# Optimization experiments

Hardware: AMD Instinct MI355X
Metric: run time of the kernel (lower is better)

Reference implementation:

```python
import jax, jax.numpy as jnp
import numpy as np

N = 40000      # nodes
E = 640000     # edges
IN_DIM = 128
HID = 128
HEADS = 4
DHEAD = HID // HEADS  # 32
LAYERS = 3
TIMESTEPS = 2
NEG_SLOPE = 0.2


def setup_inputs() -> dict:
    key = jax.random.key(0)
    ks = jax.random.split(key, 16)
    s = 0.05
    inp = {
        "node_feats": jax.random.normal(ks[0], (N, IN_DIM), jnp.float32),
        "src": jax.random.randint(ks[1], (E,), 0, N, jnp.int32),
        "dst": jax.random.randint(ks[2], (E,), 0, N, jnp.int32),
        "proj_W": jax.random.normal(ks[3], (IN_DIM, HID), jnp.float32) * s,
        "proj_b": jnp.zeros((HID,), jnp.float32),
        "fc_W": jax.random.normal(ks[4], (LAYERS, HID, HID), jnp.float32) * s,
        "attn_l": jax.random.normal(ks[5], (LAYERS, HEADS, DHEAD), jnp.float32) * s,
        "attn_r": jax.random.normal(ks[6], (LAYERS, HEADS, DHEAD), jnp.float32) * s,
        "conv_bias": jnp.zeros((LAYERS, HID), jnp.float32),
        "gru_Wih": jax.random.normal(ks[7], (3 * HID, HID), jnp.float32) * s,
        "gru_Whh": jax.random.normal(ks[8], (3 * HID, HID), jnp.float32) * s,
        "gru_bih": jnp.zeros((3 * HID,), jnp.float32),
        "gru_bhh": jnp.zeros((3 * HID,), jnp.float32),
    }
    return inp


def _gat_layer(h, src, dst, fc_W, attn_l, attn_r, bias):
    # h: (N, HID). DGL GATConv: fc -> edge attn -> segment softmax -> scatter sum
    feat = (h @ fc_W).reshape(N, HEADS, DHEAD)
    el = jnp.einsum('nhd,hd->nh', feat, attn_l)  # (N, H)
    er = jnp.einsum('nhd,hd->nh', feat, attn_r)
    e = jax.nn.leaky_relu(el[src] + er[dst], NEG_SLOPE)  # (E, H)
    # segment softmax over incoming edges per destination node
    emax = jax.ops.segment_max(e, dst, num_segments=N)  # (N, H)
    ee = jnp.exp(e - emax[dst])
    denom = jax.ops.segment_sum(ee, dst, num_segments=N)
    alpha = ee / denom[dst]  # (E, H)
    msg = feat[src] * alpha[:, :, None]  # (E, H, D)
    rst = jax.ops.segment_sum(msg, dst, num_segments=N)  # (N, H, D)
    rst = rst + h.reshape(N, HEADS, DHEAD)          # identity residual
    rst = rst + bias.reshape(HEADS, DHEAD)          # learned bias
    return jax.nn.elu(rst).reshape(N, HID)


def _gru_step(x, Wih, Whh, bih, bhh):
    # seq_len == 1, h0 == 0 -> recurrent matmul Whh @ h0 vanishes; b_hh remains
    gi = x @ Wih.T + bih  # (N, 3*HID)
    r = jax.nn.sigmoid(gi[:, :HID] + bhh[:HID])
    z = jax.nn.sigmoid(gi[:, HID:2 * HID] + bhh[HID:2 * HID])
    n = jnp.tanh(gi[:, 2 * HID:] + r * bhh[2 * HID:])
    return (1.0 - z) * n


def reference(node_feats, src, dst, proj_W, proj_b, fc_W, attn_l, attn_r,
              conv_bias, gru_Wih, gru_Whh, gru_bih, gru_bhh):
    h = node_feats @ proj_W + proj_b
    for l in range(LAYERS):
        h = _gat_layer(h, src, dst, fc_W[l], attn_l[l], attn_r[l], conv_bias[l])
    for _ in range(TIMESTEPS):
        h = _gru_step(h, gru_Wih, gru_Whh, gru_bih, gru_bhh)
    return h
```

## Files before the change

### kernel.cpp

```cpp
#include <hip/hip_runtime.h>
#include <hip/hip_bf16.h>

#define NNODES 40000
#define NEDGES 640000
#define M2PAD  40064
#define HID    128
#define PADCAP 920064

typedef __attribute__((ext_vector_type(8))) short bf16x8;
typedef __attribute__((ext_vector_type(4))) float f32x4;

__device__ __forceinline__ float bl(unsigned u){ return __uint_as_float(u << 16); }
__device__ __forceinline__ float bh(unsigned u){ return __uint_as_float(u & 0xFFFF0000u); }
__device__ __forceinline__ unsigned short f2b(float f){
    unsigned u = __float_as_uint(f);
    u = (u + 0x7FFFu + ((u >> 16) & 1u)) >> 16;
    return (unsigned short)u;
}
__device__ __forceinline__ float fast_rcp(float x){ return __builtin_amdgcn_rcpf(x); }

__device__ __forceinline__ void g2l16(const void* g, void* l){
    __builtin_amdgcn_global_load_lds(
        (const __attribute__((address_space(1))) unsigned int*)g,
        (__attribute__((address_space(3))) unsigned int*)l, 16, 0, 0);
}

__device__ __forceinline__ float wcalc(float e, float erw, int j, int rem){
    float t = e + erw;
    t = (t > 0.f) ? t : 0.2f * t;
    t = __expf(t);
    return (j < rem) ? t : 0.f;
}

__device__ __forceinline__ unsigned lds_off(int row, int col){
    return (unsigned)(row * 256 + (((col >> 3) ^ (row & 15)) << 4) + ((col & 7) << 1));
}

__global__ void prep_all(const float* __restrict__ node_feats,
                         const float* __restrict__ proj_W, const float* __restrict__ fc_W,
                         const float* __restrict__ gru_Wih, const int* __restrict__ dstp,
                         unsigned short* __restrict__ nf,
                         unsigned short* __restrict__ projWT, unsigned short* __restrict__ fcWT,
                         unsigned short* __restrict__ gruWb, int* __restrict__ deg){
    int b = blockIdx.x;
    if (b < 5000){
        int gid = b * 256 + threadIdx.x;
        float4 v = ((const float4*)node_feats)[gid];
        ushort4 o;
        o.x = f2b(v.x); o.y = f2b(v.y); o.z = f2b(v.z); o.w = f2b(v.w);
        ((ushort4*)nf)[gid] = o;
    } else if (b < 5256){
        int t = b - 5000;
        int c = t >> 6;
        int idx = (t & 63) * 256 + threadIdx.x;
        const float* in   = (c == 0) ? proj_W : fc_W + (size_t)(c - 1) * 16384;
        unsigned short* o = (c == 0) ? projWT : fcWT + (size_t)(c - 1) * 16384;
        int k = idx >> 7, n = idx & 127;
        o[n * 128 + k] = f2b(in[idx]);
    } else if (b < 5448){
        int idx = (b - 5256) * 256 + threadIdx.x;
        gruWb[idx] = f2b(gru_Wih[idx]);
    } else {
        int e = (b - 5448) * 256 + threadIdx.x;
        atomicAdd(&deg[dstp[e]], 1);
    }
}

__global__ __launch_bounds__(1024) void scan_kernel(const int* __restrict__ deg,
        int* __restrict__ rowptr, int* __restrict__ cur, int Nn4){
    __shared__ int wsum[17];
    __shared__ int carry;
    int t = threadIdx.x, lane = t & 63, wid = t >> 6;
    if (t == 0) carry = 0;
    __syncthreads();
    for (int base = 0; base < Nn4; base += 1024){
        int i4 = base + t;
        int4 dg = (i4 < Nn4) ? ((const int4*)deg)[i4] : make_int4(0, 0, 0, 0);
        int p0 = (dg.x + 7) & ~7, p1 = (dg.y + 7) & ~7;
        int p2 = (dg.z + 7) & ~7, p3 = (dg.w + 7) & ~7;
        int v = p0 + p1 + p2 + p3;
        int x = v;
        #pragma unroll
        for (int d = 1; d < 64; d <<= 1){
            int y = __shfl_up(x, d, 64);
            if (lane >= d) x += y;
        }
        if (lane == 63) wsum[wid] = x;
        __syncthreads();
        if (wid == 0){
            int vv = (lane < 16) ? wsum[lane] : 0;
            int xx = vv;
            #pragma unroll
            for (int d = 1; d < 16; d <<= 1){
                int y = __shfl_up(xx, d, 64);
                if (lane >= d) xx += y;
            }
            if (lane < 16) wsum[lane] = xx - vv;
            if (lane == 15) wsum[16] = xx;
        }
        __syncthreads();
        int excl = carry + wsum[wid] + (x - v);
        if (i4 < Nn4){
            int4 o = make_int4(excl, excl + p0, excl + p0 + p1, excl + p0 + p1 + p2);
            ((int4*)rowptr)[i4] = o;
            ((int4*)cur)[i4]    = o;
        }
        __syncthreads();
        if (t == 0) carry += wsum[16];
        __syncthreads();
    }
    if (t == 0) rowptr[Nn4 * 4] = carry;
}

__global__ void fill_kernel(const int* __restrict__ src, const int* __restrict__ dst,
                            int* __restrict__ cur, int* __restrict__ esrc){
    int e = blockIdx.x * 256 + threadIdx.x;
    int d = dst[e];
    int pos = atomicAdd(&cur[d], 1);
    esrc[pos] = src[e];
}

template<int MT>
__global__ __launch_bounds__(256) void gemm_t(
        const unsigned short* __restrict__ A, const unsigned short* __restrict__ BT,
        const float* __restrict__ bias, void* __restrict__ C,
        int Mreal, int ldc, int outF32,
        const float* __restrict__ al, const float* __restrict__ ar,
        float* __restrict__ elp, float* __restrict__ erp)
{
    __shared__ unsigned char lds[MT * 256 + 32768];
    unsigned char* ldsA = lds;
    unsigned char* ldsB = lds + MT * 256;
    int w = threadIdx.x >> 6, lane = threadIdx.x & 63;
    int rsub = lane >> 4, c16 = lane & 15;
    long baseM = (long)blockIdx.x * MT;
    long baseN = (long)blockIdx.y * 128;

    #pragma unroll
    for (int i = 0; i < MT / 16; i++){
        int chunk = w * (MT / 16) + i;
        int r = chunk * 4 + rsub;
        int cg = c16 ^ (r & 15);
        long ar_ = baseM + r; if (ar_ >= Mreal) ar_ = Mreal - 1;
        g2l16((const unsigned char*)A + ar_ * 256 + cg * 16, ldsA + chunk * 1024);
    }
    #pragma unroll
    for (int i = 0; i < 8; i++){
        int chunk = w * 8 + i;
        int r = chunk * 4 + rsub;
        int cg = c16 ^ (r & 15);
        long br = baseN + r;
        g2l16((const unsigned char*)BT + br * 256 + cg * 16, ldsB + chunk * 1024);
    }
    __syncthreads();

    constexpr int MI = 4;
    constexpr int NI = (MT == 128) ? 4 : 2;
    int mo = (MT == 128) ? (w & 1) * 64 : 0;
    int no = (MT == 128) ? (w >> 1) * 64 : w * 32;
    int q = lane >> 4, cl = lane & 15;
    f32x4 acc[MI][NI];
    #pragma unroll
    for (int i = 0; i < MI; i++)
        #pragma unroll
        for (int j = 0; j < NI; j++) acc[i][j] = (f32x4){0.f, 0.f, 0.f, 0.f};

    #pragma unroll
    for (int kc = 0; kc < 4; kc++){
        bf16x8 av[MI], bv[NI];
        #pragma unroll
        for (int mi = 0; mi < MI; mi++){
            int row = mo + mi * 16 + cl;
            int cs = (kc * 4 + q) ^ (row & 15);
            av[mi] = *(const bf16x8*)(ldsA + row * 256 + cs * 16);
        }
        #pragma unroll
        for (int ni = 0; ni < NI; ni++){
            int row = no + ni * 16 + cl;
            int cs = (kc * 4 + q) ^ (row & 15);
            bv[ni] = *(const bf16x8*)(ldsB + row * 256 + cs * 16);
        }
        #pragma unroll
        for (int mi = 0; mi < MI; mi++)
            #pragma unroll
            for (int ni = 0; ni < NI; ni++)
                acc[mi][ni] = __builtin_amdgcn_mfma_f32_16x16x32_bf16(av[mi], bv[ni], acc[mi][ni], 0, 0, 0);
    }

    #pragma unroll
    for (int mi = 0; mi < MI; mi++){
        #pragma unroll
        for (int ni = 0; ni < NI; ni++){
            int gn = (int)baseN + no + ni * 16 + cl;
            float bvf = bias ? bias[gn] : 0.f;
            long gm0 = baseM + mo + mi * 16 + q * 4;
            #pragma unroll
            for (int reg = 0; reg < 4; reg++){
                float v = acc[mi][ni][reg] + bvf;
                long gm = gm0 + reg;
                if (gm < Mreal){
                    if (outF32) ((float*)C)[gm * ldc + gn] = v;
                    else ((unsigned short*)C)[gm * ldc + gn] = f2b(v);
                }
            }
        }
    }

    if (NI == 2 && al){
        float al_lo = al[no + cl], al_hi = al[no + 16 + cl];
        float ar_lo = ar[no + cl], ar_hi = ar[no + 16 + cl];
        #pragma unroll
        for (int mi = 0; mi < MI; mi++){
            #pragma unroll
            for (int reg = 0; reg < 4; reg++){
                float pl = acc[mi][0][reg] * al_lo + acc[mi][1][reg] * al_hi;
                float pr = acc[mi][0][reg] * ar_lo + acc[mi][1][reg] * ar_hi;
                #pragma unroll
                for (int msk = 8; msk; msk >>= 1){
                    pl += __shfl_xor(pl, msk, 64);
                    pr += __shfl_xor(pr, msk, 64);
                }
                long gm = baseM + mi * 16 + q * 4 + reg;
                if (cl == 0 && gm < Mreal){
                    elp[gm * 4 + w] = pl;
                    erp[gm * 4 + w] = pr;
                }
            }
        }
    }
}

__global__ __launch_bounds__(256) void proj_fc1(
        const unsigned short* __restrict__ nf,
        const unsigned short* __restrict__ projWT, const float* __restrict__ proj_b,
        const unsigned short* __restrict__ fcWT0,
        unsigned short* __restrict__ h, unsigned short* __restrict__ feat,
        const float* __restrict__ al, const float* __restrict__ ar,
        float* __restrict__ elp, float* __restrict__ erp)
{
    __shared__ unsigned char ldsA[16384];
    __shared__ unsigned char ldsB[32768];
    int w = threadIdx.x >> 6, lane = threadIdx.x & 63;
    int rsub = lane >> 4, c16 = lane & 15;
    long baseM = (long)blockIdx.x * 64;

    #pragma unroll
    for (int i = 0; i < 4; i++){
        int chunk = w * 4 + i;
        int r = chunk * 4 + rsub;
        int cg = c16 ^ (r & 15);
        g2l16((const unsigned char*)nf + (baseM + r) * 256 + cg * 16, ldsA + chunk * 1024);
    }
    #pragma unroll
    for (int i = 0; i < 8; i++){
        int chunk = w * 8 + i;
        int r = chunk * 4 + rsub;
        int cg = c16 ^ (r & 15);
        g2l16((const unsigned char*)projWT + r * 256 + cg * 16, ldsB + chunk * 1024);
    }
    __syncthreads();

    int no = w * 32;
    int q = lane >> 4, cl = lane & 15;
    f32x4 acc[4][2];
    #pragma unroll
    for (int i = 0; i < 4; i++)
        #pragma unroll
        for (int j = 0; j < 2; j++) acc[i][j] = (f32x4){0.f, 0.f, 0.f, 0.f};

    #pragma unroll
    for (int kc = 0; kc < 4; kc++){
        bf16x8 av[4], bv[2];
        #pragma unroll
        for (int mi = 0; mi < 4; mi++){
            int row = mi * 16 + cl;
            int cs = (kc * 4 + q) ^ (row & 15);
            av[mi] = *(const bf16x8*)(ldsA + row * 256 + cs * 16);
        }
        #pragma unroll
        for (int ni = 0; ni < 2; ni++){
            int row = no + ni * 16 + cl;
            int cs = (kc * 4 + q) ^ (row & 15);
            bv[ni] = *(const bf16x8*)(ldsB + row * 256 + cs * 16);
        }
        #pragma unroll
        for (int mi = 0; mi < 4; mi++)
            #pragma unroll
            for (int ni = 0; ni < 2; ni++)
                acc[mi][ni] = __builtin_amdgcn_mfma_f32_16x16x32_bf16(av[mi], bv[ni], acc[mi][ni], 0, 0, 0);
    }
    __syncthreads();

    #pragma unroll
    for (int ni = 0; ni < 2; ni++){
        int j = no + ni * 16 + cl;
        float bvf = proj_b[j];
        #pragma unroll
        for (int mi = 0; mi < 4; mi++){
            #pragma unroll
            for (int reg = 0; reg < 4; reg++){
                int row = mi * 16 + q * 4 + reg;
                unsigned short bb = f2b(acc[mi][ni][reg] + bvf);
                h[(baseM + row) * 128 + j] = bb;
                *(unsigned short*)(ldsA + lds_off(row, j)) = bb;
            }
        }
    }
    #pragma unroll
    for (int i = 0; i < 8; i++){
        int chunk = w * 8 + i;
        int r = chunk * 4 + rsub;
        int cg = c16 ^ (r & 15);
        g2l16((const unsigned char*)fcWT0 + r * 256 + cg * 16, ldsB + chunk * 1024);
    }
    __syncthreads();

    #pragma unroll
    for (int i = 0; i < 4; i++)
        #pragma unroll
        for (int j = 0; j < 2; j++) acc[i][j] = (f32x4){0.f, 0.f, 0.f, 0.f};

    #pragma unroll
    for (int kc = 0; kc < 4; kc++){
        bf16x8 av[4], bv[2];
        #pragma unroll
        for (int mi = 0; mi < 4; mi++){
            int row = mi * 16 + cl;
            int cs = (kc * 4 + q) ^ (row & 15);
            av[mi] = *(const bf16x8*)(ldsA + row * 256 + cs * 16);
        }
        #pragma unroll
        for (int ni = 0; ni < 2; ni++){
            int row = no + ni * 16 + cl;
            int cs = (kc * 4 + q) ^ (row & 15);
            bv[ni] = *(const bf16x8*)(ldsB + row * 256 + cs * 16);
        }
        #pragma unroll
        for (int mi = 0; mi < 4; mi++)
            #pragma unroll
            for (int ni = 0; ni < 2; ni++)
                acc[mi][ni] = __builtin_amdgcn_mfma_f32_16x16x32_bf16(av[mi], bv[ni], acc[mi][ni], 0, 0, 0);
    }

    #pragma unroll
    for (int mi = 0; mi < 4; mi++){
        #pragma unroll
        for (int ni = 0; ni < 2; ni++){
            int gn = no + ni * 16 + cl;
            #pragma unroll
            for (int reg = 0; reg < 4; reg++){
                long gm = baseM + mi * 16 + q * 4 + reg;
                feat[gm * 128 + gn] = f2b(acc[mi][ni][reg]);
            }
        }
    }
    float al_lo = al[no + cl], al_hi = al[no + 16 + cl];
    float ar_lo = ar[no + cl], ar_hi = ar[no + 16 + cl];
    #pragma unroll
    for (int mi = 0; mi < 4; mi++){
        #pragma unroll
        for (int reg = 0; reg < 4; reg++){
            float pl = acc[mi][0][reg] * al_lo + acc[mi][1][reg] * al_hi;
            float pr = acc[mi][0][reg] * ar_lo + acc[mi][1][reg] * ar_hi;
            #pragma unroll
            for (int msk = 8; msk; msk >>= 1){
                pl += __shfl_xor(pl, msk, 64);
                pr += __shfl_xor(pr, msk, 64);
            }
            long gm = baseM + mi * 16 + q * 4 + reg;
            if (cl == 0){
                elp[gm * 4 + w] = pl;
                erp[gm * 4 + w] = pr;
            }
        }
    }
}

__global__ __launch_bounds__(256) void gru2x(
        const unsigned short* __restrict__ A, const unsigned short* __restrict__ BT,
        const float* __restrict__ bih, const float* __restrict__ bhh,
        float* __restrict__ out, int Mreal)
{
    __shared__ unsigned char ldsA[16384];
    __shared__ unsigned char ldsB[32768];
    int w = threadIdx.x >> 6, lane = threadIdx.x & 63;
    int rsub = lane >> 4, c16 = lane & 15;
    long baseM = (long)blockIdx.x * 64;

    #pragma unroll
    for (int i = 0; i < 4; i++){
        int chunk = w * 4 + i;
        int r = chunk * 4 + rsub;
        int cg = c16 ^ (r & 15);
        g2l16((const unsigned char*)A + (baseM + r) * 256 + cg * 16, ldsA + chunk * 1024);
    }

    int no = w * 32;
    int q = lane >> 4, cl = lane & 15;
    f32x4 acc[3][4][2];

    #pragma unroll
    for (int s = 0; s < 2; s++){
        #pragma unroll
        for (int c = 0; c < 3; c++)
            #pragma unroll
            for (int i = 0; i < 4; i++)
                #pragma unroll
                for (int j = 0; j < 2; j++) acc[c][i][j] = (f32x4){0.f, 0.f, 0.f, 0.f};

        #pragma unroll
        for (int c = 0; c < 3; c++){
            __syncthreads();
            #pragma unroll
            for (int i = 0; i < 8; i++){
                int chunk = w * 8 + i;
                int r = chunk * 4 + rsub;
                int cg = c16 ^ (r & 15);
                long br = c * 128 + r;
                g2l16((const unsigned char*)BT + br * 256 + cg * 16, ldsB + chunk * 1024);
            }
            __syncthreads();
            #pragma unroll
            for (int kc = 0; kc < 4; kc++){
                bf16x8 av[4], bv[2];
                #pragma unroll
                for (int mi = 0; mi < 4; mi++){
                    int row = mi * 16 + cl;
                    int cs = (kc * 4 + q) ^ (row & 15);
                    av[mi] = *(const bf16x8*)(ldsA + row * 256 + cs * 16);
                }
                #pragma unroll
                for (int ni = 0; ni < 2; ni++){
                    int row = no + ni * 16 + cl;
                    int cs = (kc * 4 + q) ^ (row & 15);
                    bv[ni] = *(const bf16x8*)(ldsB + row * 256 + cs * 16);
                }
                #pragma unroll
                for (int mi = 0; mi < 4; mi++)
                    #pragma unroll
                    for (int ni = 0; ni < 2; ni++)
                        acc[c][mi][ni] = __builtin_amdgcn_mfma_f32_16x16x32_bf16(av[mi], bv[ni], acc[c][mi][ni], 0, 0, 0);
            }
        }
        if (s == 0) __syncthreads();

        #pragma unroll
        for (int ni = 0; ni < 2; ni++){
            int j = no + ni * 16 + cl;
            float bir = bih[j]       + bhh[j];
            float biz = bih[128 + j] + bhh[128 + j];
            float bin = bih[256 + j];
            float bhn = bhh[256 + j];
            #pragma unroll
            for (int mi = 0; mi < 4; mi++){
                #pragma unroll
                for (int reg = 0; reg < 4; reg++){
                    int row = mi * 16 + q * 4 + reg;
                    float gr = acc[0][mi][ni][reg] + bir;
                    float gz = acc[1][mi][ni][reg] + biz;
                    float gn = acc[2][mi][ni][reg] + bin;
                    float r = fast_rcp(1.f + __expf(-gr));
                    float z = fast_rcp(1.f + __expf(-gz));
                    float ex = __expf(2.f * (gn + r * bhn));
                    float nn = (ex - 1.f) * fast_rcp(ex + 1.f);
                    float v = (1.f - z) * nn;
                    if (s == 0){
                        *(unsigned short*)(ldsA + lds_off(row, j)) = f2b(v);
                    } else {
                        long nr = baseM + row;
                        if (nr < Mreal) out[nr * 128 + j] = v;
                    }
                }
            }
        }
    }
}

__global__ __launch_bounds__(256) void aggregate(
        const int* __restrict__ rowptr, const int* __restrict__ degv,
        const int* __restrict__ esrc,
        const float* __restrict__ el, const float* __restrict__ er,
        const unsigned short* __restrict__ feat, const float* __restrict__ bias,
        unsigned short* __restrict__ h)
{
    int wid = threadIdx.x >> 6, lane = threadIdx.x & 63;
    int n = blockIdx.x * 4 + wid;
    int hh = lane >> 4;
    int d0 = lane * 2;
    unsigned doff = (unsigned)(d0 * 2);
    int beg = rowptr[n], end = rowptr[n + 1];
    int dg  = degv[n];
    float erw = er[(size_t)n * 4 + hh];
    float s = 0.f, a0 = 0.f, a1 = 0.f;
    const char* fbc = (const char*)feat;
    const int*  ep  = esrc + beg;

    if (beg < end){
        int4 sA = *(const int4*)(ep);
        int4 sB = *(const int4*)(ep + 4);
        float e0=0.f,e1=0.f,e2=0.f,e3=0.f,e4=0.f,e5=0.f,e6=0.f,e7=0.f;
        unsigned f0=0,f1=0,f2=0,f3=0,f4=0,f5=0,f6=0,f7=0;
        int rprev = 0;
        int rcur  = dg;
        for (int p = beg; p < end; p += 8){
            float g0 = el[(((unsigned)sA.x) << 2) + hh];
            float g1 = el[(((unsigned)sA.y) << 2) + hh];
            float g2 = el[(((unsigned)sA.z) << 2) + hh];
            float g3 = el[(((unsigned)sA.w) << 2) + hh];
            float g4 = el[(((unsigned)sB.x) << 2) + hh];
            float g5 = el[(((unsigned)sB.y) << 2) + hh];
            float g6 = el[(((unsigned)sB.z) << 2) + hh];
            float g7 = el[(((unsigned)sB.w) << 2) + hh];
            unsigned c0 = *(const unsigned*)(fbc + ((((unsigned)sA.x) << 8) + doff));
            unsigned c1 = *(const unsigned*)(fbc + ((((unsigned)sA.y) << 8) + doff));
            unsigned c2 = *(const unsigned*)(fbc + ((((unsigned)sA.z) << 8) + doff));
            unsigned c3 = *(const unsigned*)(fbc + ((((unsigned)sA.w) << 8) + doff));
            unsigned c4 = *(const unsigned*)(fbc + ((((unsigned)sB.x) << 8) + doff));
            unsigned c5 = *(const unsigned*)(fbc + ((((unsigned)sB.y) << 8) + doff));
            unsigned c6 = *(const unsigned*)(fbc + ((((unsigned)sB.z) << 8) + doff));
            unsigned c7 = *(const unsigned*)(fbc + ((((unsigned)sB.w) << 8) + doff));
            int4 nA = *(const int4*)(ep + 8);
            int4 nB = *(const int4*)(ep + 12);
            float w0 = wcalc(e0, erw, 0, rprev);
            float w1 = wcalc(e1, erw, 1, rprev);
            float w2 = wcalc(e2, erw, 2, rprev);
            float w3 = wcalc(e3, erw, 3, rprev);
            float w4 = wcalc(e4, erw, 4, rprev);
            float w5 = wcalc(e5, erw, 5, rprev);
            float w6 = wcalc(e6, erw, 6, rprev);
            float w7 = wcalc(e7, erw, 7, rprev);
            s += ((w0 + w1) + (w2 + w3)) + ((w4 + w5) + (w6 + w7));
            a0 = fmaf(w0, bl(f0), fmaf(w1, bl(f1), fmaf(w2, bl(f2), fmaf(w3, bl(f3), a0))));
            a0 = fmaf(w4, bl(f4), fmaf(w5, bl(f5), fmaf(w6, bl(f6), fmaf(w7, bl(f7), a0))));
            a1 = fmaf(w0, bh(f0), fmaf(w1, bh(f1), fmaf(w2, bh(f2), fmaf(w3, bh(f3), a1))));
            a1 = fmaf(w4, bh(f4), fmaf(w5, bh(f5), fmaf(w6, bh(f6), fmaf(w7, bh(f7), a1))));
            e0 = g0; e1 = g1; e2 = g2; e3 = g3; e4 = g4; e5 = g5; e6 = g6; e7 = g7;
            f0 = c0; f1 = c1; f2 = c2; f3 = c3; f4 = c4; f5 = c5; f6 = c6; f7 = c7;
            sA = nA; sB = nB;
            rprev = rcur; rcur -= 8;
            ep += 8;
        }
        float w0 = wcalc(e0, erw, 0, rprev);
        float w1 = wcalc(e1, erw, 1, rprev);
        float w2 = wcalc(e2, erw, 2, rprev);
        float w3 = wcalc(e3, erw, 3, rprev);
        float w4 = wcalc(e4, erw, 4, rprev);
        float w5 = wcalc(e5, erw, 5, rprev);
        float w6 = wcalc(e6, erw, 6, rprev);
        float w7 = wcalc(e7, erw, 7, rprev);
        s += ((w0 + w1) + (w2 + w3)) + ((w4 + w5) + (w6 + w7));
        a0 = fmaf(w0, bl(f0), fmaf(w1, bl(f1), fmaf(w2, bl(f2), fmaf(w3, bl(f3), a0))));
        a0 = fmaf(w4, bl(f4), fmaf(w5, bl(f5), fmaf(w6, bl(f6), fmaf(w7, bl(f7), a0))));
        a1 = fmaf(w0, bh(f0), fmaf(w1, bh(f1), fmaf(w2, bh(f2), fmaf(w3, bh(f3), a1))));
        a1 = fmaf(w4, bh(f4), fmaf(w5, bh(f5), fmaf(w6, bh(f6), fmaf(w7, bh(f7), a1))));
    }
    float inv = (s > 0.f) ? fast_rcp(s) : 0.f;
    unsigned hv = *(const unsigned*)(h + (size_t)n * 128 + d0);
    float x0 = a0 * inv + bl(hv) + bias[d0];
    float x1 = a1 * inv + bh(hv) + bias[d0 + 1];
    x0 = (x0 > 0.f) ? x0 : expm1f(x0);
    x1 = (x1 > 0.f) ? x1 : expm1f(x1);
    unsigned outv = (unsigned)f2b(x0) | ((unsigned)f2b(x1) << 16);
    *(unsigned*)(h + (size_t)n * 128 + d0) = outv;
}

extern "C" void kernel_launch(void* const* d_in, const int* in_sizes, int n_in,
                              void* d_out, int out_size, void* d_ws, size_t ws_size,
                              hipStream_t stream) {
    const float* node_feats = (const float*)d_in[0];
    const int*   srcp       = (const int*)d_in[1];
    const int*   dstp       = (const int*)d_in[2];
    const float* proj_W     = (const float*)d_in[3];
    const float* proj_b     = (const float*)d_in[4];
    const float* fc_W       = (const float*)d_in[5];
    const float* attn_l     = (const float*)d_in[6];
    const float* attn_r     = (const float*)d_in[7];
    const float* conv_bias  = (const float*)d_in[8];
    const float* gru_Wih    = (const float*)d_in[9];
    const float* gru_bih    = (const float*)d_in[11];
    const float* gru_bhh    = (const float*)d_in[12];
    float* outp = (float*)d_out;

    char* ws = (char*)d_ws;
    size_t off = 0;
    auto carve = [&](size_t bytes) -> char* {
        char* p = ws + off;
        off += (bytes + 255) & ~(size_t)255;
        return p;
    };
    int*            deg    = (int*)carve((size_t)NNODES * 4);
    int*            rowptr = (int*)carve((size_t)(NNODES + 1) * 4);
    int*            cur    = (int*)carve((size_t)NNODES * 4);
    int*            esrc   = (int*)carve((size_t)(PADCAP + 32) * 4);
    float*          el     = (float*)carve((size_t)NNODES * 4 * 4);
    float*          er     = (float*)carve((size_t)NNODES * 4 * 4);
    unsigned short* projWT = (unsigned short*)carve(16384 * 2);
    unsigned short* fcWT   = (unsigned short*)carve(3 * 16384 * 2);
    unsigned short* gruWb  = (unsigned short*)carve(49152 * 2);
    unsigned short* nf     = (unsigned short*)carve((size_t)NNODES * 128 * 2);
    unsigned short* h      = (unsigned short*)carve((size_t)M2PAD * 128 * 2);
    unsigned short* feat   = (unsigned short*)carve((size_t)M2PAD * 128 * 2);
    (void)ws_size; (void)in_sizes; (void)n_in; (void)out_size;

    hipMemsetAsync(deg, 0, (size_t)NNODES * 4, stream);
    hipMemsetAsync(esrc, 0, (size_t)(PADCAP + 32) * 4, stream);
    prep_all<<<7948, 256, 0, stream>>>(node_feats, proj_W, fc_W, gru_Wih, dstp,
                                       nf, projWT, fcWT, gruWb, deg);
    scan_kernel<<<1, 1024, 0, stream>>>(deg, rowptr, cur, NNODES / 4);
    fill_kernel<<<NEDGES / 256, 256, 0, stream>>>(srcp, dstp, cur, esrc);

    proj_fc1<<<625, 256, 0, stream>>>(nf, projWT, proj_b, fcWT, h, feat,
                                      attn_l, attn_r, el, er);

    for (int l = 0; l < 3; l++){
        if (l > 0){
            gemm_t<64><<<dim3(625, 1), 256, 0, stream>>>(h, fcWT + l * 16384, nullptr, feat, NNODES, 128, 0,
                                                         attn_l + l * 128, attn_r + l * 128, el, er);
        }
        aggregate<<<NNODES / 4, 256, 0, stream>>>(rowptr, deg, esrc, el, er, feat,
                                                  conv_bias + l * 128, h);
    }

    gru2x<<<625, 256, 0, stream>>>(h, gruWb, gru_bih, gru_bhh, outp, NNODES);
}
```

Measured before the change: 361.8 us.

## Split degree atomics into 8 sub-counters and load GEMM operands directly from global

Degree counting and CSR fill now spread their atomics across 8 sub-counter arrays chosen by edge index, which cuts contention on hot destination nodes. The scan merges these into per-node totals and per-slot offsets. The GEMM, proj_fc1 and GRU kernels drop the LDS staging through global_load_lds and read A and B fragments straight from global memory, removing barriers and LDS traffic at the cost of redundant, uncoalesced global reads. The two memsets are merged into one, and the row bounds checks are removed because the grid covers exactly the node count.

```diff
diff --git a/kernel.cpp b/kernel.cpp
--- a/kernel.cpp
+++ b/kernel.cpp
@@ -19,12 +19,6 @@
 }
 __device__ __forceinline__ float fast_rcp(float x){ return __builtin_amdgcn_rcpf(x); }
 
-__device__ __forceinline__ void g2l16(const void* g, void* l){
-    __builtin_amdgcn_global_load_lds(
-        (const __attribute__((address_space(1))) unsigned int*)g,
-        (__attribute__((address_space(3))) unsigned int*)l, 16, 0, 0);
-}
-
 __device__ __forceinline__ float wcalc(float e, float erw, int j, int rem){
     float t = e + erw;
     t = (t > 0.f) ? t : 0.2f * t;
@@ -41,7 +35,7 @@
                          const float* __restrict__ gru_Wih, const int* __restrict__ dstp,
                          unsigned short* __restrict__ nf,
                          unsigned short* __restrict__ projWT, unsigned short* __restrict__ fcWT,
-                         unsigned short* __restrict__ gruWb, int* __restrict__ deg){
+                         unsigned short* __restrict__ gruWb, int* __restrict__ deg8){
     int b = blockIdx.x;
     if (b < 5000){
         int gid = b * 256 + threadIdx.x;
@@ -62,12 +56,12 @@
         gruWb[idx] = f2b(gru_Wih[idx]);
     } else {
         int e = (b - 5448) * 256 + threadIdx.x;
-        atomicAdd(&deg[dstp[e]], 1);
-    }
-}
-
-__global__ __launch_bounds__(1024) void scan_kernel(const int* __restrict__ deg,
-        int* __restrict__ rowptr, int* __restrict__ cur, int Nn4){
+        atomicAdd(&deg8[(e & 7) * NNODES + dstp[e]], 1);
+    }
+}
+
+__global__ __launch_bounds__(1024) void scan_kernel(const int* __restrict__ deg8,
+        int* __restrict__ rowptr, int* __restrict__ degt, int* __restrict__ cur8, int Nn4){
     __shared__ int wsum[17];
     __shared__ int carry;
     int t = threadIdx.x, lane = t & 63, wid = t >> 6;
@@ -75,15 +69,22 @@
     __syncthreads();
     for (int base = 0; base < Nn4; base += 1024){
         int i4 = base + t;
-        int4 dg = (i4 < Nn4) ? ((const int4*)deg)[i4] : make_int4(0, 0, 0, 0);
-        int p0 = (dg.x + 7) & ~7, p1 = (dg.y + 7) & ~7;
-        int p2 = (dg.z + 7) & ~7, p3 = (dg.w + 7) & ~7;
+        int4 d[8];
+        #pragma unroll
+        for (int x = 0; x < 8; x++)
+            d[x] = (i4 < Nn4) ? ((const int4*)(deg8 + (size_t)x * NNODES))[i4]
+                              : make_int4(0, 0, 0, 0);
+        int s0 = 0, s1 = 0, s2 = 0, s3 = 0;
+        #pragma unroll
+        for (int x = 0; x < 8; x++){ s0 += d[x].x; s1 += d[x].y; s2 += d[x].z; s3 += d[x].w; }
+        int p0 = (s0 + 7) & ~7, p1 = (s1 + 7) & ~7;
+        int p2 = (s2 + 7) & ~7, p3 = (s3 + 7) & ~7;
         int v = p0 + p1 + p2 + p3;
         int x = v;
         #pragma unroll
-        for (int d = 1; d < 64; d <<= 1){
-            int y = __shfl_up(x, d, 64);
-            if (lane >= d) x += y;
+        for (int dd = 1; dd < 64; dd <<= 1){
+            int y = __shfl_up(x, dd, 64);
+            if (lane >= dd) x += y;
         }
         if (lane == 63) wsum[wid] = x;
         __syncthreads();
@@ -91,9 +92,9 @@
             int vv = (lane < 16) ? wsum[lane] : 0;
             int xx = vv;
             #pragma unroll
-            for (int d = 1; d < 16; d <<= 1){
-                int y = __shfl_up(xx, d, 64);
-                if (lane >= d) xx += y;
+            for (int dd = 1; dd < 16; dd <<= 1){
+                int y = __shfl_up(xx, dd, 64);
+                if (lane >= dd) xx += y;
             }
             if (lane < 16) wsum[lane] = xx - vv;
             if (lane == 15) wsum[16] = xx;
@@ -103,7 +104,13 @@
         if (i4 < Nn4){
             int4 o = make_int4(excl, excl + p0, excl + p0 + p1, excl + p0 + p1 + p2);
             ((int4*)rowptr)[i4] = o;
-            ((int4*)cur)[i4]    = o;
+            ((int4*)degt)[i4]   = make_int4(s0, s1, s2, s3);
+            int o0 = o.x, o1 = o.y, o2 = o.z, o3 = o.w;
+            #pragma unroll
+            for (int xx2 = 0; xx2 < 8; xx2++){
+                ((int4*)(cur8 + (size_t)xx2 * NNODES))[i4] = make_int4(o0, o1, o2, o3);
+                o0 += d[xx2].x; o1 += d[xx2].y; o2 += d[xx2].z; o3 += d[xx2].w;
+            }
         }
         __syncthreads();
         if (t == 0) carry += wsum[16];
@@ -113,118 +120,77 @@
 }
 
 __global__ void fill_kernel(const int* __restrict__ src, const int* __restrict__ dst,
-                            int* __restrict__ cur, int* __restrict__ esrc){
+                            int* __restrict__ cur8, int* __restrict__ esrc){
     int e = blockIdx.x * 256 + threadIdx.x;
     int d = dst[e];
-    int pos = atomicAdd(&cur[d], 1);
+    int pos = atomicAdd(&cur8[(e & 7) * NNODES + d], 1);
     esrc[pos] = src[e];
 }
 
-template<int MT>
 __global__ __launch_bounds__(256) void gemm_t(
         const unsigned short* __restrict__ A, const unsigned short* __restrict__ BT,
-        const float* __restrict__ bias, void* __restrict__ C,
-        int Mreal, int ldc, int outF32,
+        unsigned short* __restrict__ C,
         const float* __restrict__ al, const float* __restrict__ ar,
         float* __restrict__ elp, float* __restrict__ erp)
 {
-    __shared__ unsigned char lds[MT * 256 + 32768];
-    unsigned char* ldsA = lds;
-    unsigned char* ldsB = lds + MT * 256;
     int w = threadIdx.x >> 6, lane = threadIdx.x & 63;
-    int rsub = lane >> 4, c16 = lane & 15;
-    long baseM = (long)blockIdx.x * MT;
-    long baseN = (long)blockIdx.y * 128;
-
-    #pragma unroll
-    for (int i = 0; i < MT / 16; i++){
-        int chunk = w * (MT / 16) + i;
-        int r = chunk * 4 + rsub;
-        int cg = c16 ^ (r & 15);
-        long ar_ = baseM + r; if (ar_ >= Mreal) ar_ = Mreal - 1;
-        g2l16((const unsigned char*)A + ar_ * 256 + cg * 16, ldsA + chunk * 1024);
-    }
-    #pragma unroll
-    for (int i = 0; i < 8; i++){
-        int chunk = w * 8 + i;
-        int r = chunk * 4 + rsub;
-        int cg = c16 ^ (r & 15);
-        long br = baseN + r;
-        g2l16((const unsigned char*)BT + br * 256 + cg * 16, ldsB + chunk * 1024);
-    }
-    __syncthreads();
-
-    constexpr int MI = 4;
-    constexpr int NI = (MT == 128) ? 4 : 2;
-    int mo = (MT == 128) ? (w & 1) * 64 : 0;
-    int no = (MT == 128) ? (w >> 1) * 64 : w * 32;
+    long baseM = (long)blockIdx.x * 64;
+    int no = w * 32;
     int q = lane >> 4, cl = lane & 15;
-    f32x4 acc[MI][NI];
-    #pragma unroll
-    for (int i = 0; i < MI; i++)
-        #pragma unroll
-        for (int j = 0; j < NI; j++) acc[i][j] = (f32x4){0.f, 0.f, 0.f, 0.f};
+    const unsigned short* Ab = A + baseM * 128;
+
+    f32x4 acc[4][2];
+    #pragma unroll
+    for (int i = 0; i < 4; i++)
+        #pragma unroll
+        for (int j = 0; j < 2; j++) acc[i][j] = (f32x4){0.f, 0.f, 0.f, 0.f};
 
     #pragma unroll
     for (int kc = 0; kc < 4; kc++){
-        bf16x8 av[MI], bv[NI];
-        #pragma unroll
-        for (int mi = 0; mi < MI; mi++){
-            int row = mo + mi * 16 + cl;
-            int cs = (kc * 4 + q) ^ (row & 15);
-            av[mi] = *(const bf16x8*)(ldsA + row * 256 + cs * 16);
-        }
-        #pragma unroll
-        for (int ni = 0; ni < NI; ni++){
-            int row = no + ni * 16 + cl;
-            int cs = (kc * 4 + q) ^ (row & 15);
-            bv[ni] = *(const bf16x8*)(ldsB + row * 256 + cs * 16);
-        }
-        #pragma unroll
-        for (int mi = 0; mi < MI; mi++)
-            #pragma unroll
-            for (int ni = 0; ni < NI; ni++)
+        int co = kc * 32 + q * 8;
+        bf16x8 av[4], bv[2];
+        #pragma unroll
+        for (int mi = 0; mi < 4; mi++)
+            av[mi] = *(const bf16x8*)(Ab + (mi * 16 + cl) * 128 + co);
+        #pragma unroll
+        for (int ni = 0; ni < 2; ni++)
+            bv[ni] = *(const bf16x8*)(BT + (no + ni * 16 + cl) * 128 + co);
+        #pragma unroll
+        for (int mi = 0; mi < 4; mi++)
+            #pragma unroll
+            for (int ni = 0; ni < 2; ni++)
                 acc[mi][ni] = __builtin_amdgcn_mfma_f32_16x16x32_bf16(av[mi], bv[ni], acc[mi][ni], 0, 0, 0);
     }
 
     #pragma unroll
-    for (int mi = 0; mi < MI; mi++){
-        #pragma unroll
-        for (int ni = 0; ni < NI; ni++){
-            int gn = (int)baseN + no + ni * 16 + cl;
-            float bvf = bias ? bias[gn] : 0.f;
-            long gm0 = baseM + mo + mi * 16 + q * 4;
-            #pragma unroll
-            for (int reg = 0; reg < 4; reg++){
-                float v = acc[mi][ni][reg] + bvf;
-                long gm = gm0 + reg;
-                if (gm < Mreal){
-                    if (outF32) ((float*)C)[gm * ldc + gn] = v;
-                    else ((unsigned short*)C)[gm * ldc + gn] = f2b(v);
-                }
-            }
-        }
-    }
-
-    if (NI == 2 && al){
-        float al_lo = al[no + cl], al_hi = al[no + 16 + cl];
-        float ar_lo = ar[no + cl], ar_hi = ar[no + 16 + cl];
-        #pragma unroll
-        for (int mi = 0; mi < MI; mi++){
-            #pragma unroll
-            for (int reg = 0; reg < 4; reg++){
-                float pl = acc[mi][0][reg] * al_lo + acc[mi][1][reg] * al_hi;
-                float pr = acc[mi][0][reg] * ar_lo + acc[mi][1][reg] * ar_hi;
-                #pragma unroll
-                for (int msk = 8; msk; msk >>= 1){
-                    pl += __shfl_xor(pl, msk, 64);
-                    pr += __shfl_xor(pr, msk, 64);
-                }
-                long gm = baseM + mi * 16 + q * 4 + reg;
-                if (cl == 0 && gm < Mreal){
-                    elp[gm * 4 + w] = pl;
-                    erp[gm * 4 + w] = pr;
-                }
+    for (int mi = 0; mi < 4; mi++){
+        #pragma unroll
+        for (int ni = 0; ni < 2; ni++){
+            int gn = no + ni * 16 + cl;
+            long gm0 = baseM + mi * 16 + q * 4;
+            #pragma unroll
+            for (int reg = 0; reg < 4; reg++)
+                C[(gm0 + reg) * 128 + gn] = f2b(acc[mi][ni][reg]);
+        }
+    }
+
+    float al_lo = al[no + cl], al_hi = al[no + 16 + cl];
+    float ar_lo = ar[no + cl], ar_hi = ar[no + 16 + cl];
+    #pragma unroll
+    for (int mi = 0; mi < 4; mi++){
+        #pragma unroll
+        for (int reg = 0; reg < 4; reg++){
+            float pl = acc[mi][0][reg] * al_lo + acc[mi][1][reg] * al_hi;
+            float pr = acc[mi][0][reg] * ar_lo + acc[mi][1][reg] * ar_hi;
+            #pragma unroll
+            for (int msk = 8; msk; msk >>= 1){
+                pl += __shfl_xor(pl, msk, 64);
+                pr += __shfl_xor(pr, msk, 64);
+            }
+            long gm = baseM + mi * 16 + q * 4 + reg;
+            if (cl == 0){
+                elp[gm * 4 + w] = pl;
+                erp[gm * 4 + w] = pr;
             }
         }
     }
@@ -239,29 +205,12 @@
         float* __restrict__ elp, float* __restrict__ erp)
 {
     __shared__ unsigned char ldsA[16384];
-    __shared__ unsigned char ldsB[32768];
     int w = threadIdx.x >> 6, lane = threadIdx.x & 63;
-    int rsub = lane >> 4, c16 = lane & 15;
     long baseM = (long)blockIdx.x * 64;
-
-    #pragma unroll
-    for (int i = 0; i < 4; i++){
-        int chunk = w * 4 + i;
-        int r = chunk * 4 + rsub;
-        int cg = c16 ^ (r & 15);
-        g2l16((const unsigned char*)nf + (baseM + r) * 256 + cg * 16, ldsA + chunk * 1024);
-    }
-    #pragma unroll
-    for (int i = 0; i < 8; i++){
-        int chunk = w * 8 + i;
-        int r = chunk * 4 + rsub;
-        int cg = c16 ^ (r & 15);
-        g2l16((const unsigned char*)projWT + r * 256 + cg * 16, ldsB + chunk * 1024);
-    }
-    __syncthreads();
-
     int no = w * 32;
     int q = lane >> 4, cl = lane & 15;
+    const unsigned short* Ab = nf + baseM * 256 / 2 * 2;
+
     f32x4 acc[4][2];
     #pragma unroll
     for (int i = 0; i < 4; i++)
@@ -270,26 +219,20 @@
 
     #pragma unroll
     for (int kc = 0; kc < 4; kc++){
+        int co = kc * 32 + q * 8;
         bf16x8 av[4], bv[2];
         #pragma unroll
-        for (int mi = 0; mi < 4; mi++){
-            int row = mi * 16 + cl;
-            int cs = (kc * 4 + q) ^ (row & 15);
-            av[mi] = *(const bf16x8*)(ldsA + row * 256 + cs * 16);
-        }
-        #pragma unroll
-        for (int ni = 0; ni < 2; ni++){
-            int row = no + ni * 16 + cl;
-            int cs = (kc * 4 + q) ^ (row & 15);
-            bv[ni] = *(const bf16x8*)(ldsB + row * 256 + cs * 16);
-        }
+        for (int mi = 0; mi < 4; mi++)
+            av[mi] = *(const bf16x8*)(nf + (baseM + mi * 16 + cl) * 128 + co);
+        #pragma unroll
+        for (int ni = 0; ni < 2; ni++)
+            bv[ni] = *(const bf16x8*)(projWT + (no + ni * 16 + cl) * 128 + co);
         #pragma unroll
         for (int mi = 0; mi < 4; mi++)
             #pragma unroll
             for (int ni = 0; ni < 2; ni++)
                 acc[mi][ni] = __builtin_amdgcn_mfma_f32_16x16x32_bf16(av[mi], bv[ni], acc[mi][ni], 0, 0, 0);
     }
-    __syncthreads();
 
     #pragma unroll
     for (int ni = 0; ni < 2; ni++){
@@ -306,13 +249,6 @@
             }
         }
     }
-    #pragma unroll
-    for (int i = 0; i < 8; i++){
-        int chunk = w * 8 + i;
-        int r = chunk * 4 + rsub;
-        int cg = c16 ^ (r & 15);
-        g2l16((const unsigned char*)fcWT0 + r * 256 + cg * 16, ldsB + chunk * 1024);
-    }
     __syncthreads();
 
     #pragma unroll
@@ -322,6 +258,7 @@
 
     #pragma unroll
     for (int kc = 0; kc < 4; kc++){
+        int co = kc * 32 + q * 8;
         bf16x8 av[4], bv[2];
         #pragma unroll
         for (int mi = 0; mi < 4; mi++){
@@ -330,11 +267,8 @@
             av[mi] = *(const bf16x8*)(ldsA + row * 256 + cs * 16);
         }
         #pragma unroll
-        for (int ni = 0; ni < 2; ni++){
-            int row = no + ni * 16 + cl;
-            int cs = (kc * 4 + q) ^ (row & 15);
-            bv[ni] = *(const bf16x8*)(ldsB + row * 256 + cs * 16);
-        }
+        for (int ni = 0; ni < 2; ni++)
+            bv[ni] = *(const bf16x8*)(fcWT0 + (no + ni * 16 + cl) * 128 + co);
         #pragma unroll
         for (int mi = 0; mi < 4; mi++)
             #pragma unroll
@@ -379,70 +313,58 @@
 __global__ __launch_bounds__(256) void gru2x(
         const unsigned short* __restrict__ A, const unsigned short* __restrict__ BT,
         const float* __restrict__ bih, const float* __restrict__ bhh,
-        float* __restrict__ out, int Mreal)
+        float* __restrict__ out)
 {
     __shared__ unsigned char ldsA[16384];
-    __shared__ unsigned char ldsB[32768];
     int w = threadIdx.x >> 6, lane = threadIdx.x & 63;
-    int rsub = lane >> 4, c16 = lane & 15;
     long baseM = (long)blockIdx.x * 64;
-
-    #pragma unroll
-    for (int i = 0; i < 4; i++){
-        int chunk = w * 4 + i;
-        int r = chunk * 4 + rsub;
-        int cg = c16 ^ (r & 15);
-        g2l16((const unsigned char*)A + (baseM + r) * 256 + cg * 16, ldsA + chunk * 1024);
-    }
-
     int no = w * 32;
     int q = lane >> 4, cl = lane & 15;
-    f32x4 acc[3][4][2];
 
     #pragma unroll
     for (int s = 0; s < 2; s++){
-        #pragma unroll
-        for (int c = 0; c < 3; c++)
-            #pragma unroll
-            for (int i = 0; i < 4; i++)
+        bf16x8 avall[4][4];
+        if (s == 0){
+            #pragma unroll
+            for (int kc = 0; kc < 4; kc++)
                 #pragma unroll
-                for (int j = 0; j < 2; j++) acc[c][i][j] = (f32x4){0.f, 0.f, 0.f, 0.f};
-
-        #pragma unroll
-        for (int c = 0; c < 3; c++){
+                for (int mi = 0; mi < 4; mi++)
+                    avall[kc][mi] = *(const bf16x8*)(A + (baseM + mi * 16 + cl) * 128 + kc * 32 + q * 8);
+        } else {
             __syncthreads();
             #pragma unroll
-            for (int i = 0; i < 8; i++){
-                int chunk = w * 8 + i;
-                int r = chunk * 4 + rsub;
-                int cg = c16 ^ (r & 15);
-                long br = c * 128 + r;
-                g2l16((const unsigned char*)BT + br * 256 + cg * 16, ldsB + chunk * 1024);
-            }
-            __syncthreads();
-            #pragma unroll
-            for (int kc = 0; kc < 4; kc++){
-                bf16x8 av[4], bv[2];
+            for (int kc = 0; kc < 4; kc++)
                 #pragma unroll
                 for (int mi = 0; mi < 4; mi++){
                     int row = mi * 16 + cl;
                     int cs = (kc * 4 + q) ^ (row & 15);
-                    av[mi] = *(const bf16x8*)(ldsA + row * 256 + cs * 16);
+                    avall[kc][mi] = *(const bf16x8*)(ldsA + row * 256 + cs * 16);
                 }
+        }
+
+        f32x4 acc[3][4][2];
+        #pragma unroll
+        for (int c = 0; c < 3; c++)
+            #pragma unroll
+            for (int i = 0; i < 4; i++)
                 #pragma unroll
-                for (int ni = 0; ni < 2; ni++){
-                    int row = no + ni * 16 + cl;
-                    int cs = (kc * 4 + q) ^ (row & 15);
-                    bv[ni] = *(const bf16x8*)(ldsB + row * 256 + cs * 16);
-                }
+                for (int j = 0; j < 2; j++) acc[c][i][j] = (f32x4){0.f, 0.f, 0.f, 0.f};
+
+        #pragma unroll
+        for (int c = 0; c < 3; c++){
+            #pragma unroll
+            for (int kc = 0; kc < 4; kc++){
+                bf16x8 bv[2];
+                #pragma unroll
+                for (int ni = 0; ni < 2; ni++)
+                    bv[ni] = *(const bf16x8*)(BT + (c * 128 + no + ni * 16 + cl) * 128 + kc * 32 + q * 8);
                 #pragma unroll
                 for (int mi = 0; mi < 4; mi++)
                     #pragma unroll
                     for (int ni = 0; ni < 2; ni++)
-                        acc[c][mi][ni] = __builtin_amdgcn_mfma_f32_16x16x32_bf16(av[mi], bv[ni], acc[c][mi][ni], 0, 0, 0);
-            }
-        }
-        if (s == 0) __syncthreads();
+                        acc[c][mi][ni] = __builtin_amdgcn_mfma_f32_16x16x32_bf16(avall[kc][mi], bv[ni], acc[c][mi][ni], 0, 0, 0);
+            }
+        }
 
         #pragma unroll
         for (int ni = 0; ni < 2; ni++){
@@ -464,12 +386,10 @@
                     float ex = __expf(2.f * (gn + r * bhn));
                     float nn = (ex - 1.f) * fast_rcp(ex + 1.f);
                     float v = (1.f - z) * nn;
-                    if (s == 0){
+                    if (s == 0)
                         *(unsigned short*)(ldsA + lds_off(row, j)) = f2b(v);
-                    } else {
-                        long nr = baseM + row;
-                        if (nr < Mreal) out[nr * 128 + j] = v;
-                    }
+                    else
+                        out[(baseM + row) * 128 + j] = v;
                 }
             }
         }
@@ -588,10 +508,11 @@
         off += (bytes + 255) & ~(size_t)255;
         return p;
     };
-    int*            deg    = (int*)carve((size_t)NNODES * 4);
+    int*            deg8   = (int*)carve((size_t)8 * NNODES * 4);
+    int*            esrc   = (int*)carve((size_t)(PADCAP + 32) * 4);
     int*            rowptr = (int*)carve((size_t)(NNODES + 1) * 4);
-    int*            cur    = (int*)carve((size_t)NNODES * 4);
-    int*            esrc   = (int*)carve((size_t)(PADCAP + 32) * 4);
+    int*            degt   = (int*)carve((size_t)NNODES * 4);
+    int*            cur8   = (int*)carve((size_t)8 * NNODES * 4);
     float*          el     = (float*)carve((size_t)NNODES * 4 * 4);
     float*          er     = (float*)carve((size_t)NNODES * 4 * 4);
     unsigned short* projWT = (unsigned short*)carve(16384 * 2);
@@ -602,24 +523,23 @@
     unsigned short* feat   = (unsigned short*)carve((size_t)M2PAD * 128 * 2);
     (void)ws_size; (void)in_sizes; (void)n_in; (void)out_size;
 
-    hipMemsetAsync(deg, 0, (size_t)NNODES * 4, stream);
-    hipMemsetAsync(esrc, 0, (size_t)(PADCAP + 32) * 4, stream);
+    hipMemsetAsync(deg8, 0, (size_t)8 * NNODES * 4 + ((size_t)(PADCAP + 32) * 4 + 255 & ~(size_t)255), stream);
     prep_all<<<7948, 256, 0, stream>>>(node_feats, proj_W, fc_W, gru_Wih, dstp,
-                                       nf, projWT, fcWT, gruWb, deg);
-    scan_kernel<<<1, 1024, 0, stream>>>(deg, rowptr, cur, NNODES / 4);
-    fill_kernel<<<NEDGES / 256, 256, 0, stream>>>(srcp, dstp, cur, esrc);
+                                       nf, projWT, fcWT, gruWb, deg8);
+    scan_kernel<<<1, 1024, 0, stream>>>(deg8, rowptr, degt, cur8, NNODES / 4);
+    fill_kernel<<<NEDGES / 256, 256, 0, stream>>>(srcp, dstp, cur8, esrc);
 
     proj_fc1<<<625, 256, 0, stream>>>(nf, projWT, proj_b, fcWT, h, feat,
                                       attn_l, attn_r, el, er);
 
     for (int l = 0; l < 3; l++){
         if (l > 0){
-            gemm_t<64><<<dim3(625, 1), 256, 0, stream>>>(h, fcWT + l * 16384, nullptr, feat, NNODES, 128, 0,
-                                                         attn_l + l * 128, attn_r + l * 128, el, er);
-        }
-        aggregate<<<NNODES / 4, 256, 0, stream>>>(rowptr, deg, esrc, el, er, feat,
+            gemm_t<<<625, 256, 0, stream>>>(h, fcWT + l * 16384, feat,
+                                            attn_l + l * 128, attn_r + l * 128, el, er);
+        }
+        aggregate<<<NNODES / 4, 256, 0, stream>>>(rowptr, degt, esrc, el, er, feat,
                                                   conv_bias + l * 128, h);
     }
 
-    gru2x<<<625, 256, 0, stream>>>(h, gruWb, gru_bih, gru_bhh, outp, NNODES);
-}
+    gru2x<<<625, 256, 0, stream>>>(h, gruWb, gru_bih, gru_bhh, outp);
+}
```

Measured after the change: 388.1 us. 1.07x slower.
